# Kernel tuning notes

Hardware: AMD Instinct MI355X
Metric: run time of the kernel (lower is better)

Reference implementation:

```python
import jax, jax.numpy as jnp
import numpy as np

B, S, D = 4, 2048, 1024  # batch, seq_len, d_model == d_internal


def setup_inputs() -> dict:
    key = jax.random.key(0)
    ks = jax.random.split(key, 7)
    s = 1.0 / np.sqrt(D)  # scale weights so softmax / relu stay in a sane range
    return {
        "input_vecs": jax.random.normal(ks[0], (B, S, D), jnp.float32),
        "Wq": jax.random.normal(ks[1], (D, D), jnp.float32) * s,
        "Wk": jax.random.normal(ks[2], (D, D), jnp.float32) * s,
        "Wv": jax.random.normal(ks[3], (D, D), jnp.float32) * s,
        "W1": jax.random.normal(ks[4], (D, D), jnp.float32) * s,  # linear1: d_internal -> d_model
        "b1": jnp.zeros((D,), jnp.float32),
        "W2": jax.random.normal(ks[5], (D, D), jnp.float32) * s,  # linear2: d_model -> d_internal
        "b2": jnp.zeros((D,), jnp.float32),
    }


def reference(input_vecs, Wq, Wk, Wv, W1, b1, W2, b2):
    d_internal = Wq.shape[1]
    # single-head self-attention: Q,K,V = X @ Wq/Wk/Wv
    q = jnp.einsum("bsd,de->bse", input_vecs, Wq)
    k = jnp.einsum("bsd,de->bse", input_vecs, Wk)
    v = jnp.einsum("bsd,de->bse", input_vecs, Wv)
    scores = jnp.einsum("bqe,bke->bqk", q, k) / jnp.sqrt(jnp.asarray(d_internal, q.dtype))
    attn = jax.nn.softmax(scores, axis=-1)               # [B, S, S]
    attn_out = jnp.einsum("bqk,bke->bqe", attn, v)       # [B, S, D]
    h = attn_out + input_vecs                            # residual 1
    h = jax.nn.relu(h @ W1 + b1)                         # linear1 + relu
    out = h @ W2 + b2 + input_vecs                       # linear2 + residual 2
    return out, attn
```

## Files before the change

### kernel.cpp

```cpp
#include <hip/hip_runtime.h>
#include <hip/hip_bf16.h>

typedef unsigned short u16;
typedef unsigned int   u32;
typedef u16   u16x8 __attribute__((ext_vector_type(8)));
typedef u16   u16x4 __attribute__((ext_vector_type(4)));
typedef __bf16 bf16x8 __attribute__((ext_vector_type(8)));
typedef float f32x4 __attribute__((ext_vector_type(4)));

__device__ __forceinline__ u16 f2bf(float f) {
    u32 u = __float_as_uint(f);
    u = u + 0x7FFFu + ((u >> 16) & 1u);
    return (u16)(u >> 16);
}

__device__ __forceinline__ void gload16(const u16* g, u16* l) {
    __builtin_amdgcn_global_load_lds(
        (const __attribute__((address_space(1))) void*)g,
        (__attribute__((address_space(3))) void*)l,
        16, 0, 0);
}

__global__ __launch_bounds__(256) void cvt_x(const float* __restrict__ X,
                                             u16* __restrict__ Xb) {
    const long i = (long)(blockIdx.x * 256 + threadIdx.x) * 8;
    float4 a = *(const float4*)(X + i);
    float4 b = *(const float4*)(X + i + 4);
    u16x8 r;
    r[0] = f2bf(a.x); r[1] = f2bf(a.y); r[2] = f2bf(a.z); r[3] = f2bf(a.w);
    r[4] = f2bf(b.x); r[5] = f2bf(b.y); r[6] = f2bf(b.z); r[7] = f2bf(b.w);
    *(u16x8*)(Xb + i) = r;
}

__global__ __launch_bounds__(256) void cvt_wT(const float* __restrict__ w0,
                                              const float* __restrict__ w1,
                                              const float* __restrict__ w2,
                                              const float* __restrict__ w3,
                                              const float* __restrict__ w4,
                                              u16* __restrict__ wt) {
    const float* srcs[5] = {w0, w1, w2, w3, w4};
    const float* W = srcs[blockIdx.z];
    u16* WT = wt + (long)blockIdx.z * 1048576;
    __shared__ float t[32][33];
    const int tx = threadIdx.x, ty = threadIdx.y;
    const int n0 = blockIdx.x * 32, k0 = blockIdx.y * 32;
    #pragma unroll
    for (int r = 0; r < 4; ++r)
        t[ty + 8 * r][tx] = W[(long)(k0 + ty + 8 * r) * 1024 + n0 + tx];
    __syncthreads();
    #pragma unroll
    for (int r = 0; r < 4; ++r)
        WT[(long)(n0 + ty + 8 * r) * 1024 + k0 + tx] = f2bf(t[tx][ty + 8 * r]);
}

#define BM 128
#define BN 128
#define BK 32

enum { EPI_QKV = 0, EPI_SCALE_F32 = 2, EPI_ADDX_BF16 = 3,
       EPI_BIAS_RELU_BF16 = 4, EPI_BIAS_ADDX_F32 = 5 };

template <int EPI>
__global__ __launch_bounds__(256, 2)
void gemm_bt(const u16* __restrict__ A, const u16* __restrict__ Bt,
             void* __restrict__ Cout, void* __restrict__ CoutK,
             void* __restrict__ CoutV,
             const float* __restrict__ bias, const float* __restrict__ Xres,
             const int M, const int N, const int K,
             const long sA, const long sB, const long sC, const long sX,
             const float scale) {
    const int bz = blockIdx.z;
    const u16* Ab = A + (long)bz * sA;
    const u16* Bb = Bt + (long)bz * sB;
    const float* Xr = Xres ? Xres + (long)bz * sX : nullptr;

    const int tid  = threadIdx.x;
    const int lane = tid & 63;
    const int w    = tid >> 6;
    const int wr   = (w >> 1) * 64;
    const int wc   = (w & 1) * 64;
    const int m0   = blockIdx.x * BM;
    const int n0   = blockIdx.y * BN;

    __shared__ __align__(16) u16 As[BM * BK];
    __shared__ __align__(16) u16 Bs[BN * BK];

    f32x4 acc[4][4] = {};

    const int schunk = ((lane & 3) ^ ((lane >> 3) & 3)) * 8;
    const u16* Ag = Ab + (long)(m0 + w * 32 + (lane >> 2)) * K + schunk;
    const u16* Bg = Bb + (long)(n0 + w * 32 + (lane >> 2)) * K + schunk;
    const long r16A = 16L * K;
    u16* As0 = &As[(w * 32) * BK];
    u16* As1 = &As[(w * 32 + 16) * BK];
    u16* Bs0 = &Bs[(w * 32) * BK];
    u16* Bs1 = &Bs[(w * 32 + 16) * BK];

    const int rbase = lane & 15;
    const int koff  = (((lane >> 4) ^ ((rbase >> 1) & 3))) * 8;

    for (int kt = 0; kt < K; kt += BK) {
        gload16(Ag + kt, As0);
        gload16(Ag + kt + r16A, As1);
        gload16(Bg + kt, Bs0);
        gload16(Bg + kt + r16A, Bs1);
        __syncthreads();

        bf16x8 af[4], bfr[4];
        #pragma unroll
        for (int mi = 0; mi < 4; ++mi)
            af[mi] = *(const bf16x8*)(&As[(wr + mi * 16 + rbase) * BK + koff]);
        #pragma unroll
        for (int ni = 0; ni < 4; ++ni)
            bfr[ni] = *(const bf16x8*)(&Bs[(wc + ni * 16 + rbase) * BK + koff]);
        #pragma unroll
        for (int mi = 0; mi < 4; ++mi)
            #pragma unroll
            for (int ni = 0; ni < 4; ++ni)
                acc[mi][ni] = __builtin_amdgcn_mfma_f32_16x16x32_bf16(
                    af[mi], bfr[ni], acc[mi][ni], 0, 0, 0);
        __syncthreads();
    }

    const int colb = wc + (lane & 15);
    const int rq   = (lane >> 4) * 4;
    #pragma unroll
    for (int mi = 0; mi < 4; ++mi) {
        #pragma unroll
        for (int ni = 0; ni < 4; ++ni) {
            f32x4 v = acc[mi][ni];
            const int gr0 = m0 + wr + mi * 16 + rq;
            const int gc  = n0 + colb + ni * 16;
            if constexpr (EPI == EPI_QKV) {
                if (bz == 2) {
                    u16x4 p;
                    p[0] = f2bf(v[0]); p[1] = f2bf(v[1]);
                    p[2] = f2bf(v[2]); p[3] = f2bf(v[3]);
                    u16* C = (u16*)CoutV;
                    const long off = ((long)(gr0 >> 11)) * 2097152 +
                                     (long)gc * 2048 + (gr0 & 2047);
                    *(u16x4*)(C + off) = p;
                } else {
                    u16* C = (u16*)(bz == 0 ? Cout : CoutK);
                    #pragma unroll
                    for (int j = 0; j < 4; ++j)
                        C[(long)(gr0 + j) * N + gc] = f2bf(v[j]);
                }
            } else {
                #pragma unroll
                for (int j = 0; j < 4; ++j) {
                    const long idx = (long)(gr0 + j) * N + gc;
                    float val = v[j];
                    if constexpr (EPI == EPI_SCALE_F32) {
                        ((float*)Cout + (long)bz * sC)[idx] = val * scale;
                    } else if constexpr (EPI == EPI_ADDX_BF16) {
                        val += Xr[idx];
                        ((u16*)Cout + (long)bz * sC)[idx] = f2bf(val);
                    } else if constexpr (EPI == EPI_BIAS_RELU_BF16) {
                        val = fmaxf(val + bias[gc], 0.0f);
                        ((u16*)Cout + (long)bz * sC)[idx] = f2bf(val);
                    } else if constexpr (EPI == EPI_BIAS_ADDX_F32) {
                        ((float*)Cout + (long)bz * sC)[idx] =
                            val + bias[gc] + Xr[idx];
                    }
                }
            }
        }
    }
}

__global__ __launch_bounds__(256)
void softmax_rows(float* __restrict__ attn, u16* __restrict__ P) {
    const int row  = blockIdx.x;
    float* rp      = attn + (long)row * 2048;
    const int tid  = threadIdx.x;
    const int lane = tid & 63;
    const int w    = tid >> 6;

    float4 v0 = *(const float4*)(rp + tid * 8);
    float4 v1 = *(const float4*)(rp + tid * 8 + 4);

    float m = fmaxf(fmaxf(fmaxf(v0.x, v0.y), fmaxf(v0.z, v0.w)),
                    fmaxf(fmaxf(v1.x, v1.y), fmaxf(v1.z, v1.w)));
    #pragma unroll
    for (int o = 32; o > 0; o >>= 1) m = fmaxf(m, __shfl_xor(m, o));
    __shared__ float redm[4];
    if (lane == 0) redm[w] = m;
    __syncthreads();
    m = fmaxf(fmaxf(redm[0], redm[1]), fmaxf(redm[2], redm[3]));

    float e[8];
    e[0] = __expf(v0.x - m); e[1] = __expf(v0.y - m);
    e[2] = __expf(v0.z - m); e[3] = __expf(v0.w - m);
    e[4] = __expf(v1.x - m); e[5] = __expf(v1.y - m);
    e[6] = __expf(v1.z - m); e[7] = __expf(v1.w - m);
    float s = ((e[0] + e[1]) + (e[2] + e[3])) + ((e[4] + e[5]) + (e[6] + e[7]));
    #pragma unroll
    for (int o = 32; o > 0; o >>= 1) s += __shfl_xor(s, o);
    __shared__ float reds[4];
    if (lane == 0) reds[w] = s;
    __syncthreads();
    s = (reds[0] + reds[1]) + (reds[2] + reds[3]);
    const float inv = 1.0f / s;

    float4 o0, o1;
    o0.x = e[0] * inv; o0.y = e[1] * inv; o0.z = e[2] * inv; o0.w = e[3] * inv;
    o1.x = e[4] * inv; o1.y = e[5] * inv; o1.z = e[6] * inv; o1.w = e[7] * inv;
    *(float4*)(rp + tid * 8)     = o0;
    *(float4*)(rp + tid * 8 + 4) = o1;

    u16x8 pb;
    pb[0] = f2bf(o0.x); pb[1] = f2bf(o0.y); pb[2] = f2bf(o0.z); pb[3] = f2bf(o0.w);
    pb[4] = f2bf(o1.x); pb[5] = f2bf(o1.y); pb[6] = f2bf(o1.z); pb[7] = f2bf(o1.w);
    *(u16x8*)(P + (long)row * 2048 + tid * 8) = pb;
}

extern "C" void kernel_launch(void* const* d_in, const int* in_sizes, int n_in,
                              void* d_out, int out_size, void* d_ws, size_t ws_size,
                              hipStream_t stream) {
    const float* X  = (const float*)d_in[0];
    const float* Wq = (const float*)d_in[1];
    const float* Wk = (const float*)d_in[2];
    const float* Wv = (const float*)d_in[3];
    const float* W1 = (const float*)d_in[4];
    const float* b1 = (const float*)d_in[5];
    const float* W2 = (const float*)d_in[6];
    const float* b2 = (const float*)d_in[7];

    float* out  = (float*)d_out;
    float* attn = out + (size_t)8388608;

    char* ws = (char*)d_ws;
    u16* Xb  = (u16*)(ws);
    u16* Qb  = (u16*)(ws + (size_t)16 * 1024 * 1024);
    u16* Kb  = (u16*)(ws + (size_t)32 * 1024 * 1024);
    u16* VT  = (u16*)(ws + (size_t)48 * 1024 * 1024);
    u16* H1b = (u16*)(ws + (size_t)64 * 1024 * 1024);
    u16* WTs = (u16*)(ws + (size_t)80 * 1024 * 1024);
    u16* W1T = WTs + (size_t)3 * 1048576;
    u16* W2T = WTs + (size_t)4 * 1048576;
    u16* Pb  = Xb;
    u16* Hb  = Kb;

    cvt_x<<<4096, 256, 0, stream>>>(X, Xb);
    cvt_wT<<<dim3(32, 32, 5), dim3(32, 8), 0, stream>>>(Wq, Wk, Wv, W1, W2, WTs);

    gemm_bt<EPI_QKV><<<dim3(64, 8, 3), 256, 0, stream>>>(
        Xb, WTs, Qb, Kb, VT, nullptr, nullptr, 8192, 1024, 1024,
        0, 1048576, 0, 0, 1.0f);

    gemm_bt<EPI_SCALE_F32><<<dim3(16, 16, 4), 256, 0, stream>>>(
        Qb, Kb, attn, nullptr, nullptr, nullptr, nullptr, 2048, 2048, 1024,
        2048L * 1024, 2048L * 1024, 2048L * 2048, 0, 0.03125f);

    softmax_rows<<<8192, 256, 0, stream>>>(attn, Pb);

    gemm_bt<EPI_ADDX_BF16><<<dim3(16, 8, 4), 256, 0, stream>>>(
        Pb, VT, Hb, nullptr, nullptr, nullptr, X, 2048, 1024, 2048,
        2048L * 2048, 1024L * 2048, 2048L * 1024, 2048L * 1024, 1.0f);

    gemm_bt<EPI_BIAS_RELU_BF16><<<dim3(64, 8, 1), 256, 0, stream>>>(
        Hb, W1T, H1b, nullptr, nullptr, b1, nullptr, 8192, 1024, 1024,
        0, 0, 0, 0, 1.0f);

    gemm_bt<EPI_BIAS_ADDX_F32><<<dim3(64, 8, 1), 256, 0, stream>>>(
        H1b, W2T, out, nullptr, nullptr, b2, X, 8192, 1024, 1024,
        0, 0, 0, 0, 1.0f);
}
```

Measured before the change: 266.5 us.

## Triple-buffer GEMM LDS tiles with async prefetch two stages ahead

Turns the single-buffered K loop of the bf16 GEMM into a three-slot LDS ring. Global-to-LDS loads for tile t+2 are issued before computing tile t, and explicit vmcnt waits plus raw barriers replace the full __syncthreads. This is meant to hide global load latency behind MFMA work. LDS use triples to 48KB per block, which may limit occupancy at two blocks per CU, and the hand-written waitcnt counts must match the number of loads in flight.

```diff
diff --git a/kernel.cpp b/kernel.cpp
--- a/kernel.cpp
+++ b/kernel.cpp
@@ -20,6 +20,8 @@
         (__attribute__((address_space(3))) void*)l,
         16, 0, 0);
 }
+
+#define WAITV(N) asm volatile("s_waitcnt vmcnt(" #N ")" ::: "memory")
 
 __global__ __launch_bounds__(256) void cvt_x(const float* __restrict__ X,
                                              u16* __restrict__ Xb) {
@@ -56,6 +58,7 @@
 #define BM 128
 #define BN 128
 #define BK 32
+#define TILE (BM * BK)
 
 enum { EPI_QKV = 0, EPI_SCALE_F32 = 2, EPI_ADDX_BF16 = 3,
        EPI_BIAS_RELU_BF16 = 4, EPI_BIAS_ADDX_F32 = 5 };
@@ -82,8 +85,8 @@
     const int m0   = blockIdx.x * BM;
     const int n0   = blockIdx.y * BN;
 
-    __shared__ __align__(16) u16 As[BM * BK];
-    __shared__ __align__(16) u16 Bs[BN * BK];
+    __shared__ __align__(16) u16 As[3 * TILE];
+    __shared__ __align__(16) u16 Bs[3 * TILE];
 
     f32x4 acc[4][4] = {};
 
@@ -91,36 +94,60 @@
     const u16* Ag = Ab + (long)(m0 + w * 32 + (lane >> 2)) * K + schunk;
     const u16* Bg = Bb + (long)(n0 + w * 32 + (lane >> 2)) * K + schunk;
     const long r16A = 16L * K;
-    u16* As0 = &As[(w * 32) * BK];
-    u16* As1 = &As[(w * 32 + 16) * BK];
-    u16* Bs0 = &Bs[(w * 32) * BK];
-    u16* Bs1 = &Bs[(w * 32 + 16) * BK];
 
     const int rbase = lane & 15;
     const int koff  = (((lane >> 4) ^ ((rbase >> 1) & 3))) * 8;
 
-    for (int kt = 0; kt < K; kt += BK) {
-        gload16(Ag + kt, As0);
-        gload16(Ag + kt + r16A, As1);
-        gload16(Bg + kt, Bs0);
-        gload16(Bg + kt + r16A, Bs1);
-        __syncthreads();
-
+    const int wbase = w * 32 * BK;
+
+    #define STAGE(KT, SLOT) do {                                   \
+        u16* a0_ = &As[(SLOT) * TILE + wbase];                     \
+        u16* b0_ = &Bs[(SLOT) * TILE + wbase];                     \
+        gload16(Ag + (KT), a0_);                                   \
+        gload16(Ag + (KT) + r16A, a0_ + 16 * BK);                  \
+        gload16(Bg + (KT), b0_);                                   \
+        gload16(Bg + (KT) + r16A, b0_ + 16 * BK);                  \
+    } while (0)
+
+    const int nt = K / BK;
+    STAGE(0, 0);
+    STAGE(BK, 1);
+    int slc = 0;
+    int sls = 2;
+
+    for (int t = 0; t < nt; ++t) {
+        const int rem = nt - 1 - t;
+        if (rem >= 2) {
+            STAGE((t + 2) * BK, sls);
+            WAITV(8);
+        } else if (rem == 1) {
+            WAITV(4);
+        } else {
+            WAITV(0);
+        }
+        __builtin_amdgcn_s_barrier();
+
+        const u16* Asl = &As[slc * TILE];
+        const u16* Bsl = &Bs[slc * TILE];
         bf16x8 af[4], bfr[4];
         #pragma unroll
         for (int mi = 0; mi < 4; ++mi)
-            af[mi] = *(const bf16x8*)(&As[(wr + mi * 16 + rbase) * BK + koff]);
+            af[mi] = *(const bf16x8*)(&Asl[(wr + mi * 16 + rbase) * BK + koff]);
         #pragma unroll
         for (int ni = 0; ni < 4; ++ni)
-            bfr[ni] = *(const bf16x8*)(&Bs[(wc + ni * 16 + rbase) * BK + koff]);
+            bfr[ni] = *(const bf16x8*)(&Bsl[(wc + ni * 16 + rbase) * BK + koff]);
         #pragma unroll
         for (int mi = 0; mi < 4; ++mi)
             #pragma unroll
             for (int ni = 0; ni < 4; ++ni)
                 acc[mi][ni] = __builtin_amdgcn_mfma_f32_16x16x32_bf16(
                     af[mi], bfr[ni], acc[mi][ni], 0, 0, 0);
-        __syncthreads();
+
+        __builtin_amdgcn_s_barrier();
+        slc = (slc == 2) ? 0 : slc + 1;
+        sls = (sls == 2) ? 0 : sls + 1;
     }
+    #undef STAGE
 
     const int colb = wc + (lane & 15);
     const int rq   = (lane >> 4) * 4;
```

Result: no change. 270.2 us (+1.4%).

## Rewrite GEMM mainloop as triple-buffered 256x128x64 pipeline with 8 waves

Applied to the files above, without the earlier changes.

The bf16 GEMM kernel moves from a 128x128x32 tile with 4 waves and a single LDS buffer to a 256x128 tile with BK=64, 8 waves and a three-slot LDS ring. Global-to-LDS loads for tile t+2 are spread across four compute phases, separated by barriers and priority bumps around the MFMA clusters. The swizzle is widened to 8 chunks to match. This is meant to hide global load latency and raise MFMA utilisation, at the cost of more LDS (about 144KB), one block per CU, fewer blocks per grid, and many extra barriers per K-step.

```diff
diff --git a/kernel.cpp b/kernel.cpp
--- a/kernel.cpp
+++ b/kernel.cpp
@@ -20,6 +20,10 @@
         (__attribute__((address_space(3))) void*)l,
         16, 0, 0);
 }
+
+#define WAITV(N) asm volatile("s_waitcnt vmcnt(" #N ")" ::: "memory")
+#define SCHEDB() __builtin_amdgcn_sched_barrier(0)
+#define BAR()    __builtin_amdgcn_s_barrier()
 
 __global__ __launch_bounds__(256) void cvt_x(const float* __restrict__ X,
                                              u16* __restrict__ Xb) {
@@ -53,15 +57,18 @@
         WT[(long)(n0 + ty + 8 * r) * 1024 + k0 + tx] = f2bf(t[tx][ty + 8 * r]);
 }
 
-#define BM 128
+#define BM 256
 #define BN 128
-#define BK 32
+#define BKW 64
+#define SLOT_A (BM * BKW)
+#define SLOT_B (BN * BKW)
+#define SLOTSZ (SLOT_A + SLOT_B)
 
 enum { EPI_QKV = 0, EPI_SCALE_F32 = 2, EPI_ADDX_BF16 = 3,
        EPI_BIAS_RELU_BF16 = 4, EPI_BIAS_ADDX_F32 = 5 };
 
 template <int EPI>
-__global__ __launch_bounds__(256, 2)
+__global__ __launch_bounds__(512, 1)
 void gemm_bt(const u16* __restrict__ A, const u16* __restrict__ Bt,
              void* __restrict__ Cout, void* __restrict__ CoutK,
              void* __restrict__ CoutV,
@@ -77,59 +84,141 @@
     const int tid  = threadIdx.x;
     const int lane = tid & 63;
     const int w    = tid >> 6;
-    const int wr   = (w >> 1) * 64;
-    const int wc   = (w & 1) * 64;
+    const int wrg  = (w >> 1) * 64;
+    const int wcg  = (w & 1) * 64;
     const int m0   = blockIdx.x * BM;
     const int n0   = blockIdx.y * BN;
 
-    __shared__ __align__(16) u16 As[BM * BK];
-    __shared__ __align__(16) u16 Bs[BN * BK];
+    __shared__ __align__(16) u16 LDS[3 * SLOTSZ];
 
     f32x4 acc[4][4] = {};
 
-    const int schunk = ((lane & 3) ^ ((lane >> 3) & 3)) * 8;
-    const u16* Ag = Ab + (long)(m0 + w * 32 + (lane >> 2)) * K + schunk;
-    const u16* Bg = Bb + (long)(n0 + w * 32 + (lane >> 2)) * K + schunk;
-    const long r16A = 16L * K;
-    u16* As0 = &As[(w * 32) * BK];
-    u16* As1 = &As[(w * 32 + 16) * BK];
-    u16* Bs0 = &Bs[(w * 32) * BK];
-    u16* Bs1 = &Bs[(w * 32 + 16) * BK];
+    const long Kl = K;
+    const int schunk = ((lane & 7) ^ (lane >> 3)) * 8;
+    const u16* Ag = Ab + (long)(m0 + w * 32 + (lane >> 3)) * Kl + schunk;
+    const u16* Bg = Bb + (long)(n0 + w * 16 + (lane >> 3)) * Kl + schunk;
 
     const int rbase = lane & 15;
-    const int koff  = (((lane >> 4) ^ ((rbase >> 1) & 3))) * 8;
-
-    for (int kt = 0; kt < K; kt += BK) {
-        gload16(Ag + kt, As0);
-        gload16(Ag + kt + r16A, As1);
-        gload16(Bg + kt, Bs0);
-        gload16(Bg + kt + r16A, Bs1);
-        __syncthreads();
-
-        bf16x8 af[4], bfr[4];
-        #pragma unroll
-        for (int mi = 0; mi < 4; ++mi)
-            af[mi] = *(const bf16x8*)(&As[(wr + mi * 16 + rbase) * BK + koff]);
-        #pragma unroll
-        for (int ni = 0; ni < 4; ++ni)
-            bfr[ni] = *(const bf16x8*)(&Bs[(wc + ni * 16 + rbase) * BK + koff]);
-        #pragma unroll
-        for (int mi = 0; mi < 4; ++mi)
-            #pragma unroll
-            for (int ni = 0; ni < 4; ++ni)
-                acc[mi][ni] = __builtin_amdgcn_mfma_f32_16x16x32_bf16(
-                    af[mi], bfr[ni], acc[mi][ni], 0, 0, 0);
-        __syncthreads();
+    const int rx    = rbase & 7;
+    const int q4    = lane >> 4;
+
+    const int dAoff = (w * 32) * BKW;
+    const int dBoff = SLOT_A + (w * 16) * BKW;
+
+    #define LDA(mi, ks) (*(const bf16x8*)(Asl + (wrg + (mi) * 16 + rbase) * BKW \
+                         + ((((ks) * 4 + q4) ^ rx)) * 8))
+    #define LDB(ni, ks) (*(const bf16x8*)(Bsl + (wcg + (ni) * 16 + rbase) * BKW \
+                         + ((((ks) * 4 + q4) ^ rx)) * 8))
+
+    const int nt = K / BKW;
+    {
+        u16* d0 = &LDS[0];
+        gload16(Ag, d0 + dAoff);
+        gload16(Ag + 8 * Kl,  d0 + dAoff + 512);
+        gload16(Ag + 16 * Kl, d0 + dAoff + 1024);
+        gload16(Ag + 24 * Kl, d0 + dAoff + 1536);
+        gload16(Bg, d0 + dBoff);
+        gload16(Bg + 8 * Kl,  d0 + dBoff + 512);
+        u16* d1 = &LDS[SLOTSZ];
+        gload16(Ag + BKW, d1 + dAoff);
+        gload16(Ag + BKW + 8 * Kl,  d1 + dAoff + 512);
+        gload16(Ag + BKW + 16 * Kl, d1 + dAoff + 1024);
+        gload16(Ag + BKW + 24 * Kl, d1 + dAoff + 1536);
+        gload16(Bg + BKW, d1 + dBoff);
+        gload16(Bg + BKW + 8 * Kl,  d1 + dBoff + 512);
     }
-
-    const int colb = wc + (lane & 15);
+    WAITV(6);
+    BAR();
+
+    int s = 0;
+    for (int t = 0; t < nt; ++t) {
+        const u16* Asl = &LDS[s * SLOTSZ];
+        const u16* Bsl = &LDS[s * SLOTSZ + SLOT_A];
+        const int s2 = (s + 2 >= 3) ? s - 1 : s + 2;
+        u16* dA = &LDS[s2 * SLOTSZ] + dAoff;
+        u16* dB = &LDS[s2 * SLOTSZ] + dBoff;
+        const bool st = (t + 2 < nt);
+        const long kt2 = (long)(t + 2) * BKW;
+
+        bf16x8 af0, af1, bf0, bf1, bf2, bf3;
+
+        if (st) { gload16(Ag + kt2, dA); gload16(Ag + kt2 + 8 * Kl, dA + 512); }
+        af0 = LDA(0, 0); af1 = LDA(1, 0);
+        bf0 = LDB(0, 0); bf1 = LDB(1, 0); bf2 = LDB(2, 0); bf3 = LDB(3, 0);
+        SCHEDB(); BAR();
+        __builtin_amdgcn_s_setprio(1);
+        acc[0][0] = __builtin_amdgcn_mfma_f32_16x16x32_bf16(af0, bf0, acc[0][0], 0, 0, 0);
+        acc[0][1] = __builtin_amdgcn_mfma_f32_16x16x32_bf16(af0, bf1, acc[0][1], 0, 0, 0);
+        acc[0][2] = __builtin_amdgcn_mfma_f32_16x16x32_bf16(af0, bf2, acc[0][2], 0, 0, 0);
+        acc[0][3] = __builtin_amdgcn_mfma_f32_16x16x32_bf16(af0, bf3, acc[0][3], 0, 0, 0);
+        acc[1][0] = __builtin_amdgcn_mfma_f32_16x16x32_bf16(af1, bf0, acc[1][0], 0, 0, 0);
+        acc[1][1] = __builtin_amdgcn_mfma_f32_16x16x32_bf16(af1, bf1, acc[1][1], 0, 0, 0);
+        acc[1][2] = __builtin_amdgcn_mfma_f32_16x16x32_bf16(af1, bf2, acc[1][2], 0, 0, 0);
+        acc[1][3] = __builtin_amdgcn_mfma_f32_16x16x32_bf16(af1, bf3, acc[1][3], 0, 0, 0);
+        __builtin_amdgcn_s_setprio(0);
+        SCHEDB(); BAR();
+
+        if (st) { gload16(Ag + kt2 + 16 * Kl, dA + 1024);
+                  gload16(Ag + kt2 + 24 * Kl, dA + 1536); }
+        af0 = LDA(2, 0); af1 = LDA(3, 0);
+        SCHEDB(); BAR();
+        __builtin_amdgcn_s_setprio(1);
+        acc[2][0] = __builtin_amdgcn_mfma_f32_16x16x32_bf16(af0, bf0, acc[2][0], 0, 0, 0);
+        acc[2][1] = __builtin_amdgcn_mfma_f32_16x16x32_bf16(af0, bf1, acc[2][1], 0, 0, 0);
+        acc[2][2] = __builtin_amdgcn_mfma_f32_16x16x32_bf16(af0, bf2, acc[2][2], 0, 0, 0);
+        acc[2][3] = __builtin_amdgcn_mfma_f32_16x16x32_bf16(af0, bf3, acc[2][3], 0, 0, 0);
+        acc[3][0] = __builtin_amdgcn_mfma_f32_16x16x32_bf16(af1, bf0, acc[3][0], 0, 0, 0);
+        acc[3][1] = __builtin_amdgcn_mfma_f32_16x16x32_bf16(af1, bf1, acc[3][1], 0, 0, 0);
+        acc[3][2] = __builtin_amdgcn_mfma_f32_16x16x32_bf16(af1, bf2, acc[3][2], 0, 0, 0);
+        acc[3][3] = __builtin_amdgcn_mfma_f32_16x16x32_bf16(af1, bf3, acc[3][3], 0, 0, 0);
+        __builtin_amdgcn_s_setprio(0);
+        SCHEDB(); BAR();
+
+        if (st) { gload16(Bg + kt2, dB); gload16(Bg + kt2 + 8 * Kl, dB + 512); }
+        af0 = LDA(0, 1); af1 = LDA(1, 1);
+        bf0 = LDB(0, 1); bf1 = LDB(1, 1); bf2 = LDB(2, 1); bf3 = LDB(3, 1);
+        SCHEDB(); BAR();
+        __builtin_amdgcn_s_setprio(1);
+        acc[0][0] = __builtin_amdgcn_mfma_f32_16x16x32_bf16(af0, bf0, acc[0][0], 0, 0, 0);
+        acc[0][1] = __builtin_amdgcn_mfma_f32_16x16x32_bf16(af0, bf1, acc[0][1], 0, 0, 0);
+        acc[0][2] = __builtin_amdgcn_mfma_f32_16x16x32_bf16(af0, bf2, acc[0][2], 0, 0, 0);
+        acc[0][3] = __builtin_amdgcn_mfma_f32_16x16x32_bf16(af0, bf3, acc[0][3], 0, 0, 0);
+        acc[1][0] = __builtin_amdgcn_mfma_f32_16x16x32_bf16(af1, bf0, acc[1][0], 0, 0, 0);
+        acc[1][1] = __builtin_amdgcn_mfma_f32_16x16x32_bf16(af1, bf1, acc[1][1], 0, 0, 0);
+        acc[1][2] = __builtin_amdgcn_mfma_f32_16x16x32_bf16(af1, bf2, acc[1][2], 0, 0, 0);
+        acc[1][3] = __builtin_amdgcn_mfma_f32_16x16x32_bf16(af1, bf3, acc[1][3], 0, 0, 0);
+        __builtin_amdgcn_s_setprio(0);
+        SCHEDB(); BAR();
+
+        af0 = LDA(2, 1); af1 = LDA(3, 1);
+        SCHEDB(); BAR();
+        __builtin_amdgcn_s_setprio(1);
+        acc[2][0] = __builtin_amdgcn_mfma_f32_16x16x32_bf16(af0, bf0, acc[2][0], 0, 0, 0);
+        acc[2][1] = __builtin_amdgcn_mfma_f32_16x16x32_bf16(af0, bf1, acc[2][1], 0, 0, 0);
+        acc[2][2] = __builtin_amdgcn_mfma_f32_16x16x32_bf16(af0, bf2, acc[2][2], 0, 0, 0);
+        acc[2][3] = __builtin_amdgcn_mfma_f32_16x16x32_bf16(af0, bf3, acc[2][3], 0, 0, 0);
+        acc[3][0] = __builtin_amdgcn_mfma_f32_16x16x32_bf16(af1, bf0, acc[3][0], 0, 0, 0);
+        acc[3][1] = __builtin_amdgcn_mfma_f32_16x16x32_bf16(af1, bf1, acc[3][1], 0, 0, 0);
+        acc[3][2] = __builtin_amdgcn_mfma_f32_16x16x32_bf16(af1, bf2, acc[3][2], 0, 0, 0);
+        acc[3][3] = __builtin_amdgcn_mfma_f32_16x16x32_bf16(af1, bf3, acc[3][3], 0, 0, 0);
+        __builtin_amdgcn_s_setprio(0);
+        SCHEDB();
+        if (st) { WAITV(6); } else { WAITV(0); }
+        BAR();
+
+        s = (s == 2) ? 0 : s + 1;
+    }
+    #undef LDA
+    #undef LDB
+
+    const int colb = wcg + (lane & 15);
     const int rq   = (lane >> 4) * 4;
     #pragma unroll
     for (int mi = 0; mi < 4; ++mi) {
         #pragma unroll
         for (int ni = 0; ni < 4; ++ni) {
             f32x4 v = acc[mi][ni];
-            const int gr0 = m0 + wr + mi * 16 + rq;
+            const int gr0 = m0 + wrg + mi * 16 + rq;
             const int gc  = n0 + colb + ni * 16;
             if constexpr (EPI == EPI_QKV) {
                 if (bz == 2) {
@@ -245,25 +334,25 @@
     cvt_x<<<4096, 256, 0, stream>>>(X, Xb);
     cvt_wT<<<dim3(32, 32, 5), dim3(32, 8), 0, stream>>>(Wq, Wk, Wv, W1, W2, WTs);
 
-    gemm_bt<EPI_QKV><<<dim3(64, 8, 3), 256, 0, stream>>>(
+    gemm_bt<EPI_QKV><<<dim3(32, 8, 3), 512, 0, stream>>>(
         Xb, WTs, Qb, Kb, VT, nullptr, nullptr, 8192, 1024, 1024,
         0, 1048576, 0, 0, 1.0f);
 
-    gemm_bt<EPI_SCALE_F32><<<dim3(16, 16, 4), 256, 0, stream>>>(
+    gemm_bt<EPI_SCALE_F32><<<dim3(8, 16, 4), 512, 0, stream>>>(
         Qb, Kb, attn, nullptr, nullptr, nullptr, nullptr, 2048, 2048, 1024,
         2048L * 1024, 2048L * 1024, 2048L * 2048, 0, 0.03125f);
 
     softmax_rows<<<8192, 256, 0, stream>>>(attn, Pb);
 
-    gemm_bt<EPI_ADDX_BF16><<<dim3(16, 8, 4), 256, 0, stream>>>(
+    gemm_bt<EPI_ADDX_BF16><<<dim3(8, 8, 4), 512, 0, stream>>>(
         Pb, VT, Hb, nullptr, nullptr, nullptr, X, 2048, 1024, 2048,
         2048L * 2048, 1024L * 2048, 2048L * 1024, 2048L * 1024, 1.0f);
 
-    gemm_bt<EPI_BIAS_RELU_BF16><<<dim3(64, 8, 1), 256, 0, stream>>>(
+    gemm_bt<EPI_BIAS_RELU_BF16><<<dim3(32, 8, 1), 512, 0, stream>>>(
         Hb, W1T, H1b, nullptr, nullptr, b1, nullptr, 8192, 1024, 1024,
         0, 0, 0, 0, 1.0f);
 
-    gemm_bt<EPI_BIAS_ADDX_F32><<<dim3(64, 8, 1), 256, 0, stream>>>(
+    gemm_bt<EPI_BIAS_ADDX_F32><<<dim3(32, 8, 1), 512, 0, stream>>>(
         H1b, W2T, out, nullptr, nullptr, b2, X, 8192, 1024, 1024,
         0, 0, 0, 0, 1.0f);
 }
```

Result: faster. 254.2 us (-4.6%).

## Triple-buffer GEMM LDS with async prefetch and grouped block swizzle

Applied to the files above, without the earlier changes.

Replaces the single-buffered GEMM main loop with a three-slot LDS ring. Global-to-LDS loads are issued two k-tiles ahead, and waits use vmcnt counters plus one barrier per iteration, so memory latency overlaps with MFMA work. Blocks are also remapped into groups of eight along M for better L2 reuse, and the occupancy hint rises to 3 blocks per CU. The LDS swizzle pattern changes to match. In exchange, LDS use triples to 48KB per block, which may limit occupancy, and the hand-written waitcnt logic must stay correct.

```diff
diff --git a/kernel.cpp b/kernel.cpp
--- a/kernel.cpp
+++ b/kernel.cpp
@@ -20,6 +20,10 @@
         (__attribute__((address_space(3))) void*)l,
         16, 0, 0);
 }
+
+#define WAITV(N) asm volatile("s_waitcnt vmcnt(" #N ")" ::: "memory")
+#define SCHEDB() __builtin_amdgcn_sched_barrier(0)
+#define BAR()    __builtin_amdgcn_s_barrier()
 
 __global__ __launch_bounds__(256) void cvt_x(const float* __restrict__ X,
                                              u16* __restrict__ Xb) {
@@ -53,23 +57,31 @@
         WT[(long)(n0 + ty + 8 * r) * 1024 + k0 + tx] = f2bf(t[tx][ty + 8 * r]);
 }
 
+enum { EPI_QKV = 0, EPI_SCALE_F32 = 2, EPI_ADDX_BF16 = 3,
+       EPI_BIAS_RELU_BF16 = 4, EPI_BIAS_ADDX_F32 = 5 };
+
 #define BM 128
 #define BN 128
 #define BK 32
-
-enum { EPI_QKV = 0, EPI_SCALE_F32 = 2, EPI_ADDX_BF16 = 3,
-       EPI_BIAS_RELU_BF16 = 4, EPI_BIAS_ADDX_F32 = 5 };
+#define SLOT_A (BM * BK)
+#define SLOTSZ (2 * SLOT_A)
 
 template <int EPI>
-__global__ __launch_bounds__(256, 2)
-void gemm_bt(const u16* __restrict__ A, const u16* __restrict__ Bt,
+__global__ __launch_bounds__(256, 3)
+void gemm128(const u16* __restrict__ A, const u16* __restrict__ Bt,
              void* __restrict__ Cout, void* __restrict__ CoutK,
              void* __restrict__ CoutV,
              const float* __restrict__ bias, const float* __restrict__ Xres,
              const int M, const int N, const int K,
              const long sA, const long sB, const long sC, const long sX,
              const float scale) {
-    const int bz = blockIdx.z;
+    const int GX = gridDim.x, GY = gridDim.y;
+    const int p  = blockIdx.x + GX * (blockIdx.y + GY * blockIdx.z);
+    const int slab = (p & 7) + 8 * (p / (8 * GY));
+    const int vy   = (p >> 3) % GY;
+    const int vx   = slab % GX;
+    const int bz   = slab / GX;
+
     const u16* Ab = A + (long)bz * sA;
     const u16* Bb = Bt + (long)bz * sB;
     const float* Xr = Xres ? Xres + (long)bz * sX : nullptr;
@@ -77,69 +89,92 @@
     const int tid  = threadIdx.x;
     const int lane = tid & 63;
     const int w    = tid >> 6;
-    const int wr   = (w >> 1) * 64;
-    const int wc   = (w & 1) * 64;
-    const int m0   = blockIdx.x * BM;
-    const int n0   = blockIdx.y * BN;
-
-    __shared__ __align__(16) u16 As[BM * BK];
-    __shared__ __align__(16) u16 Bs[BN * BK];
+    const int wrg  = (w >> 1) * 64;
+    const int wcg  = (w & 1) * 64;
+    const int m0   = vx * BM;
+    const int n0   = vy * BN;
+
+    __shared__ __align__(16) u16 LDS[3 * SLOTSZ];
 
     f32x4 acc[4][4] = {};
 
-    const int schunk = ((lane & 3) ^ ((lane >> 3) & 3)) * 8;
-    const u16* Ag = Ab + (long)(m0 + w * 32 + (lane >> 2)) * K + schunk;
-    const u16* Bg = Bb + (long)(n0 + w * 32 + (lane >> 2)) * K + schunk;
-    const long r16A = 16L * K;
-    u16* As0 = &As[(w * 32) * BK];
-    u16* As1 = &As[(w * 32 + 16) * BK];
-    u16* Bs0 = &Bs[(w * 32) * BK];
-    u16* Bs1 = &Bs[(w * 32 + 16) * BK];
+    const long Kl = K;
+    const int schunk = ((lane & 3) ^ ((lane >> 2) & 3)) * 8;
+    const u16* Ag = Ab + (long)(m0 + w * 32 + (lane >> 2)) * Kl + schunk;
+    const u16* Bg = Bb + (long)(n0 + w * 32 + (lane >> 2)) * Kl + schunk;
 
     const int rbase = lane & 15;
-    const int koff  = (((lane >> 4) ^ ((rbase >> 1) & 3))) * 8;
-
-    for (int kt = 0; kt < K; kt += BK) {
-        gload16(Ag + kt, As0);
-        gload16(Ag + kt + r16A, As1);
-        gload16(Bg + kt, Bs0);
-        gload16(Bg + kt + r16A, Bs1);
-        __syncthreads();
-
-        bf16x8 af[4], bfr[4];
+    const int koff  = ((lane >> 4) ^ (rbase & 3)) * 8;
+
+    const int dAoff = (w * 32) * BK;
+    const int dBoff = SLOT_A + (w * 32) * BK;
+
+    #define LDA(mi) (*(const bf16x8*)(Asl + (wrg + (mi) * 16 + rbase) * BK + koff))
+    #define LDB(ni) (*(const bf16x8*)(Bsl + (wcg + (ni) * 16 + rbase) * BK + koff))
+    #define STAGE(KT, SLOT) do {                                   \
+        u16* a_ = &LDS[(SLOT) * SLOTSZ + dAoff];                   \
+        u16* b_ = &LDS[(SLOT) * SLOTSZ + dBoff];                   \
+        gload16(Ag + (KT), a_);                                    \
+        gload16(Ag + (KT) + 16 * Kl, a_ + 512);                    \
+        gload16(Bg + (KT), b_);                                    \
+        gload16(Bg + (KT) + 16 * Kl, b_ + 512);                    \
+    } while (0)
+
+    const int nt = K / BK;
+    STAGE(0, 0);
+    STAGE(BK, 1);
+    WAITV(4);
+    BAR();
+
+    int s = 0;
+    for (int t = 0; t < nt; ++t) {
+        const u16* Asl = &LDS[s * SLOTSZ];
+        const u16* Bsl = &LDS[s * SLOTSZ + SLOT_A];
+        const int s2 = (s + 2 >= 3) ? s - 1 : s + 2;
+        const bool st = (t + 2 < nt);
+
+        if (st) STAGE((long)(t + 2) * BK, s2);
+
+        bf16x8 af[4], bf[4];
         #pragma unroll
-        for (int mi = 0; mi < 4; ++mi)
-            af[mi] = *(const bf16x8*)(&As[(wr + mi * 16 + rbase) * BK + koff]);
+        for (int mi = 0; mi < 4; ++mi) af[mi] = LDA(mi);
         #pragma unroll
-        for (int ni = 0; ni < 4; ++ni)
-            bfr[ni] = *(const bf16x8*)(&Bs[(wc + ni * 16 + rbase) * BK + koff]);
+        for (int ni = 0; ni < 4; ++ni) bf[ni] = LDB(ni);
         #pragma unroll
         for (int mi = 0; mi < 4; ++mi)
             #pragma unroll
             for (int ni = 0; ni < 4; ++ni)
                 acc[mi][ni] = __builtin_amdgcn_mfma_f32_16x16x32_bf16(
-                    af[mi], bfr[ni], acc[mi][ni], 0, 0, 0);
-        __syncthreads();
+                    af[mi], bf[ni], acc[mi][ni], 0, 0, 0);
+
+        SCHEDB();
+        if (st) { WAITV(4); } else { WAITV(0); }
+        BAR();
+        SCHEDB();
+        s = (s == 2) ? 0 : s + 1;
     }
-
-    const int colb = wc + (lane & 15);
+    #undef LDA
+    #undef LDB
+    #undef STAGE
+
+    const int colb = wcg + (lane & 15);
     const int rq   = (lane >> 4) * 4;
     #pragma unroll
     for (int mi = 0; mi < 4; ++mi) {
         #pragma unroll
         for (int ni = 0; ni < 4; ++ni) {
             f32x4 v = acc[mi][ni];
-            const int gr0 = m0 + wr + mi * 16 + rq;
+            const int gr0 = m0 + wrg + mi * 16 + rq;
             const int gc  = n0 + colb + ni * 16;
             if constexpr (EPI == EPI_QKV) {
                 if (bz == 2) {
-                    u16x4 p;
-                    p[0] = f2bf(v[0]); p[1] = f2bf(v[1]);
-                    p[2] = f2bf(v[2]); p[3] = f2bf(v[3]);
+                    u16x4 p2;
+                    p2[0] = f2bf(v[0]); p2[1] = f2bf(v[1]);
+                    p2[2] = f2bf(v[2]); p2[3] = f2bf(v[3]);
                     u16* C = (u16*)CoutV;
                     const long off = ((long)(gr0 >> 11)) * 2097152 +
                                      (long)gc * 2048 + (gr0 & 2047);
-                    *(u16x4*)(C + off) = p;
+                    *(u16x4*)(C + off) = p2;
                 } else {
                     u16* C = (u16*)(bz == 0 ? Cout : CoutK);
                     #pragma unroll
@@ -245,25 +280,25 @@
     cvt_x<<<4096, 256, 0, stream>>>(X, Xb);
     cvt_wT<<<dim3(32, 32, 5), dim3(32, 8), 0, stream>>>(Wq, Wk, Wv, W1, W2, WTs);
 
-    gemm_bt<EPI_QKV><<<dim3(64, 8, 3), 256, 0, stream>>>(
+    gemm128<EPI_QKV><<<dim3(64, 8, 3), 256, 0, stream>>>(
         Xb, WTs, Qb, Kb, VT, nullptr, nullptr, 8192, 1024, 1024,
         0, 1048576, 0, 0, 1.0f);
 
-    gemm_bt<EPI_SCALE_F32><<<dim3(16, 16, 4), 256, 0, stream>>>(
+    gemm128<EPI_SCALE_F32><<<dim3(16, 16, 4), 256, 0, stream>>>(
         Qb, Kb, attn, nullptr, nullptr, nullptr, nullptr, 2048, 2048, 1024,
         2048L * 1024, 2048L * 1024, 2048L * 2048, 0, 0.03125f);
 
     softmax_rows<<<8192, 256, 0, stream>>>(attn, Pb);
 
-    gemm_bt<EPI_ADDX_BF16><<<dim3(16, 8, 4), 256, 0, stream>>>(
+    gemm128<EPI_ADDX_BF16><<<dim3(16, 8, 4), 256, 0, stream>>>(
         Pb, VT, Hb, nullptr, nullptr, nullptr, X, 2048, 1024, 2048,
         2048L * 2048, 1024L * 2048, 2048L * 1024, 2048L * 1024, 1.0f);
 
-    gemm_bt<EPI_BIAS_RELU_BF16><<<dim3(64, 8, 1), 256, 0, stream>>>(
+    gemm128<EPI_BIAS_RELU_BF16><<<dim3(64, 8, 1), 256, 0, stream>>>(
         Hb, W1T, H1b, nullptr, nullptr, b1, nullptr, 8192, 1024, 1024,
         0, 0, 0, 0, 1.0f);
 
-    gemm_bt<EPI_BIAS_ADDX_F32><<<dim3(64, 8, 1), 256, 0, stream>>>(
+    gemm128<EPI_BIAS_ADDX_F32><<<dim3(64, 8, 1), 256, 0, stream>>>(
         H1b, W2T, out, nullptr, nullptr, b2, X, 8192, 1024, 1024,
         0, 0, 0, 0, 1.0f);
 }
```

After: 261.5 us. Within noise of the previous version (-1.8%).
